# Optimization experiments

Hardware: AMD Instinct MI355X
Metric: run time of the kernel (lower is better)

Reference implementation:

```python
import jax, jax.numpy as jnp
import numpy as np

B, T, D, MP = 32, 256, 512, 20


def setup_inputs() -> dict:
    key = jax.random.key(0)
    k1, k2, k3 = jax.random.split(key, 3)
    reps_lt = jax.random.normal(k1, (B, T, D), dtype=jnp.float32)
    reps_rt = jax.random.normal(k2, (B, T, D), dtype=jnp.float32)
    kernel = jax.random.normal(k3, (1, 1, 1, MP, D), dtype=jnp.float32)
    return {"reps_lt": reps_lt, "reps_rt": reps_rt, "kernel": kernel}


def reference(reps_lt, reps_rt, kernel):
    # kernel: (1,1,1,m,d) -> (m,d)
    km = kernel.reshape(kernel.shape[-2], kernel.shape[-1])
    # scores[b,t,s,m] = sum_d lt[b,t,d] * km[m,d] * rt[b,s,d]
    # matches original broadcast-multiply + sum over d (cosine_norm=False path)
    scores = jnp.einsum('btd,md,bsd->btsm', reps_lt, km, reps_rt)
    match = jnp.tanh(scores)               # [b, t1, t2, m]
    return jnp.max(match, axis=2)          # max-pool over t2 -> [b, t1, m]
```

## Files before the change

kernel.cpp:

```cpp
#include <hip/hip_runtime.h>


constexpr int TT = 256;
constexpr int DD = 512;
constexpr int NM = 20;
constexpr int NB = 32;
constexpr int BM = 64;
constexpr int NK = 4;

typedef float f32x4 __attribute__((ext_vector_type(4)));
typedef int   i32x8 __attribute__((ext_vector_type(8)));

__device__ __forceinline__ unsigned pack_bf16(float lo, float hi) {
    unsigned ulo = __builtin_bit_cast(unsigned, lo);
    unsigned uhi = __builtin_bit_cast(unsigned, hi);
    return (ulo >> 16) | (uhi & 0xFFFF0000u);
}

__device__ __forceinline__ unsigned pk4_fp8(float a, float b, float c, float d) {
    unsigned r = __builtin_amdgcn_cvt_pk_fp8_f32(a, b, 0, false);
    return __builtin_amdgcn_cvt_pk_fp8_f32(c, d, r, true);
}

__device__ __forceinline__ float blo(unsigned u) { return __builtin_bit_cast(float, u << 16); }
__device__ __forceinline__ float bhi(unsigned u) { return __builtin_bit_cast(float, u); }

__device__ __forceinline__ i32x8 mk8(uint4 a, uint4 b) {
    i32x8 v;
    v[0] = (int)a.x; v[1] = (int)a.y; v[2] = (int)a.z; v[3] = (int)a.w;
    v[4] = (int)b.x; v[5] = (int)b.y; v[6] = (int)b.z; v[7] = (int)b.w;
    return v;
}

__global__ __launch_bounds__(256)
void cast_inputs(const float* __restrict__ lt, const float* __restrict__ rt,
                 unsigned short* __restrict__ ltb, unsigned char* __restrict__ rtf)
{
    const int half = (int)gridDim.x >> 1;
    if ((int)blockIdx.x < half) {
        size_t base = ((size_t)blockIdx.x * 256 + threadIdx.x) * 8;
        float4 a = *(const float4*)(lt + base);
        float4 b = *(const float4*)(lt + base + 4);
        uint4 w;
        w.x = pack_bf16(a.x, a.y);
        w.y = pack_bf16(a.z, a.w);
        w.z = pack_bf16(b.x, b.y);
        w.w = pack_bf16(b.z, b.w);
        *(uint4*)(ltb + base) = w;
    } else {
        size_t base = ((size_t)(blockIdx.x - half) * 256 + threadIdx.x) * 8;
        float4 a = *(const float4*)(rt + base);
        float4 b = *(const float4*)(rt + base + 4);
        uint2 o;
        o.x = pk4_fp8(a.x, a.y, a.z, a.w);
        o.y = pk4_fp8(b.x, b.y, b.z, b.w);
        *(uint2*)(rtf + base) = o;
    }
}

__global__ __launch_bounds__(256, 2)
void mp_match_mx(const unsigned short* __restrict__ ltb, const unsigned char* __restrict__ rtf,
                 const float* __restrict__ km, float* __restrict__ out)
{
    __shared__ __attribute__((aligned(16))) uint4 Ash[BM * 33];
    __shared__ __attribute__((aligned(16))) float maxbuf[4][BM];

    const int f  = blockIdx.x;
    const int c8 = f & 7;
    const int i  = f >> 3;
    const int b  = c8 + 8 * (i / 80);
    const int j  = i % 80;
    const int m  = j >> 2;
    const int t0 = (j & 3) * BM;

    const int tid  = threadIdx.x;
    const int w    = tid >> 6;
    const int lane = tid & 63;
    const int l15  = lane & 15;
    const int l4   = lane >> 4;
    const int ws   = w * 64;

    const unsigned short* ltB = ltb + ((size_t)b * TT + t0) * DD;
    const unsigned char*  rtB = rtf + (size_t)b * TT * DD;
    const float*          kmp = km  + (size_t)m * DD;

    auto loadB = [&](int kk, uint4* d) {
#pragma unroll
        for (int jj = 0; jj < 4; ++jj) {
            const unsigned char* p = rtB + (size_t)(ws + jj * 16 + l15) * DD + kk * 128 + l4 * 32;
            d[jj * 2]     = *(const uint4*)p;
            d[jj * 2 + 1] = *(const uint4*)(p + 16);
        }
    };

    uint4 b0[8], b1[8];
    loadB(0, b0);

    const int cc = tid & 31, r0 = (tid >> 5) * 8;
    const float4 kA = *(const float4*)(kmp + cc * 16);
    const float4 kB = *(const float4*)(kmp + cc * 16 + 4);
    const float4 kC = *(const float4*)(kmp + cc * 16 + 8);
    const float4 kD = *(const float4*)(kmp + cc * 16 + 12);
#pragma unroll
    for (int r = 0; r < 8; ++r) {
        const unsigned short* src = ltB + (size_t)(r0 + r) * DD + cc * 16;
        uint4 h0 = *(const uint4*)src;
        uint4 h1 = *(const uint4*)(src + 8);
        uint4 o;
        o.x = pk4_fp8(blo(h0.x) * kA.x, bhi(h0.x) * kA.y, blo(h0.y) * kA.z, bhi(h0.y) * kA.w);
        o.y = pk4_fp8(blo(h0.z) * kB.x, bhi(h0.z) * kB.y, blo(h0.w) * kB.z, bhi(h0.w) * kB.w);
        o.z = pk4_fp8(blo(h1.x) * kC.x, bhi(h1.x) * kC.y, blo(h1.y) * kC.z, bhi(h1.y) * kC.w);
        o.w = pk4_fp8(blo(h1.z) * kD.x, bhi(h1.z) * kD.y, blo(h1.w) * kD.z, bhi(h1.w) * kD.w);
        Ash[(r0 + r) * 33 + cc] = o;
    }
    __syncthreads();

    auto loadA = [&](int kk, uint4* d) {
#pragma unroll
        for (int ii = 0; ii < 4; ++ii) {
            int base = (ii * 16 + l15) * 33 + kk * 8 + l4 * 2;
            d[ii * 2]     = Ash[base];
            d[ii * 2 + 1] = Ash[base + 1];
        }
    };

    f32x4 acc[4][4] = {};
    uint4 aA[8], aB[8];
    loadA(0, aA);

#pragma unroll
    for (int kk = 0; kk < NK; ++kk) {
        uint4* bc = (kk & 1) ? b1 : b0;
        uint4* bn = (kk & 1) ? b0 : b1;
        const uint4* ac = (kk & 1) ? aB : aA;
        uint4* an = (kk & 1) ? aA : aB;
        if (kk + 1 < NK) {
            loadB(kk + 1, bn);
            loadA(kk + 1, an);
        }
        i32x8 av[4], bv[4];
#pragma unroll
        for (int ii = 0; ii < 4; ++ii) av[ii] = mk8(ac[ii * 2], ac[ii * 2 + 1]);
#pragma unroll
        for (int jj = 0; jj < 4; ++jj) bv[jj] = mk8(bc[jj * 2], bc[jj * 2 + 1]);
#pragma unroll
        for (int ii = 0; ii < 4; ++ii)
#pragma unroll
            for (int jj = 0; jj < 4; ++jj)
                acc[ii][jj] = __builtin_amdgcn_mfma_scale_f32_16x16x128_f8f6f4(
                    av[ii], bv[jj], acc[ii][jj], 0, 0, 0, 127, 0, 127);
    }

#pragma unroll
    for (int ii = 0; ii < 4; ++ii) {
        f32x4 v = acc[ii][0];
#pragma unroll
        for (int jj = 1; jj < 4; ++jj) {
            v.x = fmaxf(v.x, acc[ii][jj].x);
            v.y = fmaxf(v.y, acc[ii][jj].y);
            v.z = fmaxf(v.z, acc[ii][jj].z);
            v.w = fmaxf(v.w, acc[ii][jj].w);
        }
#pragma unroll
        for (int off = 1; off < 16; off <<= 1) {
            v.x = fmaxf(v.x, __shfl_xor(v.x, off, 64));
            v.y = fmaxf(v.y, __shfl_xor(v.y, off, 64));
            v.z = fmaxf(v.z, __shfl_xor(v.z, off, 64));
            v.w = fmaxf(v.w, __shfl_xor(v.w, off, 64));
        }
        if (l15 == 0)
            *(f32x4*)&maxbuf[w][ii * 16 + l4 * 4] = v;
    }
    __syncthreads();
    if (tid < BM) {
        float v = fmaxf(fmaxf(maxbuf[0][tid], maxbuf[1][tid]),
                        fmaxf(maxbuf[2][tid], maxbuf[3][tid]));
        out[((size_t)b * TT + t0 + tid) * NM + m] = tanhf(v);
    }
}

typedef short bf16x8 __attribute__((ext_vector_type(8)));

__global__ __launch_bounds__(256, 2)
void mp_match_kernel(const float* __restrict__ lt, const float* __restrict__ rt,
                     const float* __restrict__ km, float* __restrict__ out)
{
    __shared__ __attribute__((aligned(16))) unsigned short Ash[2][4][128][8];
    __shared__ __attribute__((aligned(16))) unsigned short Bsh2[2][4][256][8];
    __shared__ __attribute__((aligned(16))) float maxbuf[2][128];

    const int ttile = blockIdx.x, m = blockIdx.y, b = blockIdx.z;
    const int t0 = ttile * 128;
    const int tid = threadIdx.x, wave = tid >> 6, lane = tid & 63;
    const int l15 = lane & 15, l4 = lane >> 4;
    const int wt = (wave & 1) * 64, wsi = wave >> 1;

    const float* ltp = lt + ((size_t)b * TT + t0) * DD;
    const float* rtp = rt + (size_t)b * TT * DD;
    const float* kmp = km + (size_t)m * DD;
    const int a_t = tid >> 1, a_h = tid & 1;

    f32x4 acc[4][8] = {};

    auto stage = [&](int kk, int buf) {
        const int d0 = kk * 32;
        const float* ap = ltp + (size_t)a_t * DD + d0 + a_h * 16;
        const float* kp = kmp + d0 + a_h * 16;
#pragma unroll
        for (int q = 0; q < 2; ++q) {
            float4 x0 = *(const float4*)(ap + q * 8);
            float4 x1 = *(const float4*)(ap + q * 8 + 4);
            float4 k0 = *(const float4*)(kp + q * 8);
            float4 k1 = *(const float4*)(kp + q * 8 + 4);
            uint4 wv;
            wv.x = pack_bf16(x0.x * k0.x, x0.y * k0.y);
            wv.y = pack_bf16(x0.z * k0.z, x0.w * k0.w);
            wv.z = pack_bf16(x1.x * k1.x, x1.y * k1.y);
            wv.w = pack_bf16(x1.z * k1.z, x1.w * k1.w);
            *(uint4*)&Ash[buf][a_h * 2 + q][a_t][0] = wv;
        }
        const float* bp = rtp + (size_t)tid * DD + d0;
#pragma unroll
        for (int p = 0; p < 4; ++p) {
            float4 y0 = *(const float4*)(bp + p * 8);
            float4 y1 = *(const float4*)(bp + p * 8 + 4);
            uint4 wv;
            wv.x = pack_bf16(y0.x, y0.y);
            wv.y = pack_bf16(y0.z, y0.w);
            wv.z = pack_bf16(y1.x, y1.y);
            wv.w = pack_bf16(y1.z, y1.w);
            *(uint4*)&Bsh2[buf][p][tid][0] = wv;
        }
    };

    stage(0, 0);
    for (int kk = 0; kk < 16; ++kk) {
        const int buf = kk & 1;
        __syncthreads();
        bf16x8 af[4], bfv[8];
#pragma unroll
        for (int i2 = 0; i2 < 4; ++i2)
            af[i2] = *(const bf16x8*)&Ash[buf][l4][wt + i2 * 16 + l15][0];
#pragma unroll
        for (int j2 = 0; j2 < 8; ++j2)
            bfv[j2] = *(const bf16x8*)&Bsh2[buf][l4][wsi * 128 + j2 * 16 + l15][0];
        if (kk + 1 < 16) stage(kk + 1, buf ^ 1);
#pragma unroll
        for (int i2 = 0; i2 < 4; ++i2)
#pragma unroll
            for (int j2 = 0; j2 < 8; ++j2)
                acc[i2][j2] = __builtin_amdgcn_mfma_f32_16x16x32_bf16(af[i2], bfv[j2], acc[i2][j2], 0, 0, 0);
    }
#pragma unroll
    for (int i2 = 0; i2 < 4; ++i2) {
        f32x4 v = acc[i2][0];
#pragma unroll
        for (int j2 = 1; j2 < 8; ++j2) {
            v.x = fmaxf(v.x, acc[i2][j2].x); v.y = fmaxf(v.y, acc[i2][j2].y);
            v.z = fmaxf(v.z, acc[i2][j2].z); v.w = fmaxf(v.w, acc[i2][j2].w);
        }
#pragma unroll
        for (int off = 1; off < 16; off <<= 1) {
            v.x = fmaxf(v.x, __shfl_xor(v.x, off, 64));
            v.y = fmaxf(v.y, __shfl_xor(v.y, off, 64));
            v.z = fmaxf(v.z, __shfl_xor(v.z, off, 64));
            v.w = fmaxf(v.w, __shfl_xor(v.w, off, 64));
        }
        if (l15 == 0) *(f32x4*)&maxbuf[wsi][wt + i2 * 16 + l4 * 4] = v;
    }
    __syncthreads();
    if (tid < 128) {
        float v = fmaxf(maxbuf[0][tid], maxbuf[1][tid]);
        out[((size_t)b * TT + t0 + tid) * NM + m] = tanhf(v);
    }
}

extern "C" void kernel_launch(void* const* d_in, const int* in_sizes, int n_in,
                              void* d_out, int out_size, void* d_ws, size_t ws_size,
                              hipStream_t stream) {
    const float* lt  = (const float*)d_in[0];
    const float* rt  = (const float*)d_in[1];
    const float* km  = (const float*)d_in[2];
    float*       out = (float*)d_out;

    const size_t elems = (size_t)NB * TT * DD;
    const size_t ltbB  = elems * sizeof(unsigned short);
    const size_t rtfB  = elems;

    if (ws_size >= ltbB + rtfB) {
        unsigned short* ltb = (unsigned short*)d_ws;
        unsigned char*  rtf = (unsigned char*)((char*)d_ws + ltbB);
        cast_inputs<<<4096, 256, 0, stream>>>(lt, rt, ltb, rtf);
        mp_match_mx<<<2560, 256, 0, stream>>>(ltb, rtf, km, out);
    } else {
        mp_match_kernel<<<dim3(2, NM, NB), 256, 0, stream>>>(lt, rt, km, out);
    }
}
```

Before: 123.8 us.

## Stream B fragments through a 4-deep ring to cut registers and raise occupancy

Replaces the double-buffered full K-slice B and A register arrays with a rolling 4-entry ring of B fragments, one 16-column fragment loaded per step with three-step lookahead. A fragments are reloaded from LDS once per K slice instead of being double-buffered. The lower register footprint allows launch bounds to rise from 2 to 3 workgroups per CU, aiming to hide global load latency through occupancy rather than software double-buffering. In exchange, each A reload must finish before the next MFMAs can use it, so latency hiding is shorter and the loads are more finely serialized.

Result: no change. 124.2 us (+0.3%).

```diff
diff --git a/kernel.cpp b/kernel.cpp
--- a/kernel.cpp
+++ b/kernel.cpp
@@ -6,7 +6,7 @@
 constexpr int NM = 20;
 constexpr int NB = 32;
 constexpr int BM = 64;
-constexpr int NK = 4;
+constexpr int NT = 16;
 
 typedef float f32x4 __attribute__((ext_vector_type(4)));
 typedef int   i32x8 __attribute__((ext_vector_type(8)));
@@ -24,13 +24,6 @@
 
 __device__ __forceinline__ float blo(unsigned u) { return __builtin_bit_cast(float, u << 16); }
 __device__ __forceinline__ float bhi(unsigned u) { return __builtin_bit_cast(float, u); }
-
-__device__ __forceinline__ i32x8 mk8(uint4 a, uint4 b) {
-    i32x8 v;
-    v[0] = (int)a.x; v[1] = (int)a.y; v[2] = (int)a.z; v[3] = (int)a.w;
-    v[4] = (int)b.x; v[5] = (int)b.y; v[6] = (int)b.z; v[7] = (int)b.w;
-    return v;
-}
 
 __global__ __launch_bounds__(256)
 void cast_inputs(const float* __restrict__ lt, const float* __restrict__ rt,
@@ -58,7 +51,7 @@
     }
 }
 
-__global__ __launch_bounds__(256, 2)
+__global__ __launch_bounds__(256, 3)
 void mp_match_mx(const unsigned short* __restrict__ ltb, const unsigned char* __restrict__ rtf,
                  const float* __restrict__ km, float* __restrict__ out)
 {
@@ -84,71 +77,63 @@
     const unsigned char*  rtB = rtf + (size_t)b * TT * DD;
     const float*          kmp = km  + (size_t)m * DD;
 
-    auto loadB = [&](int kk, uint4* d) {
-#pragma unroll
-        for (int jj = 0; jj < 4; ++jj) {
-            const unsigned char* p = rtB + (size_t)(ws + jj * 16 + l15) * DD + kk * 128 + l4 * 32;
-            d[jj * 2]     = *(const uint4*)p;
-            d[jj * 2 + 1] = *(const uint4*)(p + 16);
-        }
+    const unsigned char* bBase = rtB + (size_t)(ws + l15) * DD + l4 * 32;
+    auto loadBj = [&](int t, i32x8* dst) {
+        const unsigned char* p = bBase + (size_t)(t & 3) * 16 * DD + (t >> 2) * 128;
+        ((uint4*)dst)[0] = *(const uint4*)p;
+        ((uint4*)dst)[1] = *(const uint4*)(p + 16);
     };
 
-    uint4 b0[8], b1[8];
-    loadB(0, b0);
-
-    const int cc = tid & 31, r0 = (tid >> 5) * 8;
-    const float4 kA = *(const float4*)(kmp + cc * 16);
-    const float4 kB = *(const float4*)(kmp + cc * 16 + 4);
-    const float4 kC = *(const float4*)(kmp + cc * 16 + 8);
-    const float4 kD = *(const float4*)(kmp + cc * 16 + 12);
-#pragma unroll
-    for (int r = 0; r < 8; ++r) {
-        const unsigned short* src = ltB + (size_t)(r0 + r) * DD + cc * 16;
-        uint4 h0 = *(const uint4*)src;
-        uint4 h1 = *(const uint4*)(src + 8);
-        uint4 o;
-        o.x = pk4_fp8(blo(h0.x) * kA.x, bhi(h0.x) * kA.y, blo(h0.y) * kA.z, bhi(h0.y) * kA.w);
-        o.y = pk4_fp8(blo(h0.z) * kB.x, bhi(h0.z) * kB.y, blo(h0.w) * kB.z, bhi(h0.w) * kB.w);
-        o.z = pk4_fp8(blo(h1.x) * kC.x, bhi(h1.x) * kC.y, blo(h1.y) * kC.z, bhi(h1.y) * kC.w);
-        o.w = pk4_fp8(blo(h1.z) * kD.x, bhi(h1.z) * kD.y, blo(h1.w) * kD.z, bhi(h1.w) * kD.w);
-        Ash[(r0 + r) * 33 + cc] = o;
+    i32x8 bv[4];
+    loadBj(0, &bv[0]);
+    loadBj(1, &bv[1]);
+
+    {
+        const int cc = tid & 31, r0 = (tid >> 5) * 8;
+        const float4 kA = *(const float4*)(kmp + cc * 16);
+        const float4 kB = *(const float4*)(kmp + cc * 16 + 4);
+        const float4 kC = *(const float4*)(kmp + cc * 16 + 8);
+        const float4 kD = *(const float4*)(kmp + cc * 16 + 12);
+#pragma unroll
+        for (int r = 0; r < 8; ++r) {
+            const unsigned short* src = ltB + (size_t)(r0 + r) * DD + cc * 16;
+            uint4 h0 = *(const uint4*)src;
+            uint4 h1 = *(const uint4*)(src + 8);
+            uint4 o;
+            o.x = pk4_fp8(blo(h0.x) * kA.x, bhi(h0.x) * kA.y, blo(h0.y) * kA.z, bhi(h0.y) * kA.w);
+            o.y = pk4_fp8(blo(h0.z) * kB.x, bhi(h0.z) * kB.y, blo(h0.w) * kB.z, bhi(h0.w) * kB.w);
+            o.z = pk4_fp8(blo(h1.x) * kC.x, bhi(h1.x) * kC.y, blo(h1.y) * kC.z, bhi(h1.y) * kC.w);
+            o.w = pk4_fp8(blo(h1.z) * kD.x, bhi(h1.z) * kD.y, blo(h1.w) * kD.z, bhi(h1.w) * kD.w);
+            Ash[(r0 + r) * 33 + cc] = o;
+        }
     }
     __syncthreads();
 
-    auto loadA = [&](int kk, uint4* d) {
+    loadBj(2, &bv[2]);
+
+    auto loadA = [&](int kk, i32x8* dst) {
 #pragma unroll
         for (int ii = 0; ii < 4; ++ii) {
             int base = (ii * 16 + l15) * 33 + kk * 8 + l4 * 2;
-            d[ii * 2]     = Ash[base];
-            d[ii * 2 + 1] = Ash[base + 1];
+            ((uint4*)&dst[ii])[0] = Ash[base];
+            ((uint4*)&dst[ii])[1] = Ash[base + 1];
         }
     };
 
     f32x4 acc[4][4] = {};
-    uint4 aA[8], aB[8];
-    loadA(0, aA);
-
-#pragma unroll
-    for (int kk = 0; kk < NK; ++kk) {
-        uint4* bc = (kk & 1) ? b1 : b0;
-        uint4* bn = (kk & 1) ? b0 : b1;
-        const uint4* ac = (kk & 1) ? aB : aA;
-        uint4* an = (kk & 1) ? aA : aB;
-        if (kk + 1 < NK) {
-            loadB(kk + 1, bn);
-            loadA(kk + 1, an);
-        }
-        i32x8 av[4], bv[4];
-#pragma unroll
-        for (int ii = 0; ii < 4; ++ii) av[ii] = mk8(ac[ii * 2], ac[ii * 2 + 1]);
-#pragma unroll
-        for (int jj = 0; jj < 4; ++jj) bv[jj] = mk8(bc[jj * 2], bc[jj * 2 + 1]);
+    i32x8 av[4];
+    loadA(0, av);
+
+#pragma unroll
+    for (int t = 0; t < NT; ++t) {
+        if (t + 3 < NT) loadBj(t + 3, &bv[(t + 3) & 3]);
+        const int jj = t & 3;
 #pragma unroll
         for (int ii = 0; ii < 4; ++ii)
-#pragma unroll
-            for (int jj = 0; jj < 4; ++jj)
-                acc[ii][jj] = __builtin_amdgcn_mfma_scale_f32_16x16x128_f8f6f4(
-                    av[ii], bv[jj], acc[ii][jj], 0, 0, 0, 127, 0, 127);
+            acc[ii][jj] = __builtin_amdgcn_mfma_scale_f32_16x16x128_f8f6f4(
+                av[ii], bv[jj], acc[ii][jj], 0, 0, 0, 127, 0, 127);
+        if (jj == 3 && t + 1 < NT)
+            loadA((t >> 2) + 1, av);
     }
 
 #pragma unroll
```
